# Kernel tuning notes

Hardware: AMD Instinct MI355X
Metric: run time of the kernel (lower is better)

Reference implementation:

```python
import jax, jax.numpy as jnp
import numpy as np

DIM = 1024
HEAD_DIM = 128
NUM_HEADS = 8
T = 8192
ATTN_SCALE = 0.1  # yarn.attn_scale after reset()
RMS_EPS = 1.1920929e-07  # torch F.rms_norm default eps for fp32


def setup_inputs() -> dict:
    key = jax.random.key(0)
    ks = jax.random.split(key, 6)
    x = jax.random.normal(ks[0], (1, T, DIM), jnp.float32)
    qkvo_w = jax.random.normal(ks[1], (4 * DIM, DIM), jnp.float32) * (DIM ** -0.5)
    ve = jax.random.normal(ks[2], (1, T, DIM), jnp.float32)
    sa_lambdas = jnp.array([0.9, 1.1], jnp.float32)
    attn_gate_w = jax.random.normal(ks[3], (NUM_HEADS, 12), jnp.float32) * 0.1
    ve_gate_w = jax.random.normal(ks[4], (NUM_HEADS, 12), jnp.float32) * 0.1
    # YaRN rotary factors, exactly as Yarn.reset()
    n_freq = HEAD_DIM // 4
    ang = (1.0 / 1024.0) ** jnp.linspace(0.0, 1.0, n_freq, dtype=jnp.float32)
    ang = jnp.repeat(ang, 2)                                   # [head_dim//2]
    ang = jnp.concatenate([ang, jnp.zeros(HEAD_DIM // 2, jnp.float32)])
    theta = jnp.arange(T, dtype=jnp.float32)[:, None] * ang[None, :]
    sign = jnp.where(jnp.arange(HEAD_DIM) % 2 == 1, -1.0, 1.0).astype(jnp.float32)
    factor1 = jnp.cos(theta)
    factor2 = jnp.sin(theta) * sign                            # odd lanes negated
    seqlens = jnp.array([0, 2048, 4096, 6144, 8192], jnp.int32)  # cu_seqlens
    return {"x": x, "qkvo_w": qkvo_w, "ve": ve, "sa_lambdas": sa_lambdas,
            "factor1": factor1, "factor2": factor2,
            "attn_gate_w": attn_gate_w, "ve_gate_w": ve_gate_w,
            "seqlens": seqlens, "bm_size": 128, "key_offset": 1}


def _rms_norm(x):
    return x * jax.lax.rsqrt(jnp.mean(x * x, axis=-1, keepdims=True) + RMS_EPS)


def _rotary(x, f1, f2):
    # x: [B, T, H, D]; pairwise flip of adjacent lanes, then f1*x + f2*flip(x)
    xf = x.reshape(*x.shape[:-1], x.shape[-1] // 2, 2)[..., ::-1].reshape(x.shape)
    return f1[None, :x.shape[1], None, :] * x + f2[None, :x.shape[1], None, :] * xf


def _windowed_varlen_attn(q, k, v, seqlens, bs, scale):
    # q,k,v: [T, H, D]; causal sliding window (bs left, 0 right), varlen via cu_seqlens.
    Tt, H, D = q.shape
    nb = Tt // bs
    pad = jnp.zeros((bs, H, D), q.dtype)
    kp = jnp.concatenate([pad, k], axis=0)
    vp = jnp.concatenate([pad, v], axis=0)
    idx = jnp.arange(nb)[:, None] * bs + jnp.arange(2 * bs)[None, :]   # [nb, 2bs] into padded
    kb, vb = kp[idx], vp[idx]                                          # [nb, 2bs, H, D]
    qb = q.reshape(nb, bs, H, D)
    gq = jnp.arange(Tt).reshape(nb, bs)                                # global query idx
    gk = idx - bs                                                      # global key idx (may be <0)
    seg = jnp.searchsorted(seqlens, jnp.arange(Tt), side='right')      # segment id per token
    sq = seg.reshape(nb, bs)
    sk = seg[jnp.clip(gk, 0, Tt - 1)]
    mask = ((gk[:, None, :] >= 0)
            & (gk[:, None, :] <= gq[:, :, None])
            & (gq[:, :, None] - gk[:, None, :] <= bs)
            & (sq[:, :, None] == sk[:, None, :]))                      # [nb, bs, 2bs]
    s = jnp.einsum('nqhd,nkhd->nhqk', qb, kb) * scale
    s = jnp.where(mask[:, None], s, -jnp.inf)
    p = jax.nn.softmax(s, axis=-1)
    return jnp.einsum('nhqk,nkhd->nqhd', p, vb).reshape(Tt, H, D)


def _forward(x, qkvo_w, ve, sa_lambdas, factor1, factor2, attn_gate_w, ve_gate_w,
             seqlens, bm_size, key_offset):
    B, Tt = x.shape[0], x.shape[1]
    H, D = NUM_HEADS, HEAD_DIM
    qkv = x @ (sa_lambdas[0] * qkvo_w[:3 * DIM]).T                    # [B, T, 3*dim]
    qkv = qkv.reshape(B, Tt, 3 * H, D)
    q, k, v = qkv[:, :, :H], qkv[:, :, H:2 * H], qkv[:, :, 2 * H:]
    q, k = _rms_norm(q), _rms_norm(k)
    q, k = _rotary(q, factor1, factor2), _rotary(k, factor1, factor2)
    if key_offset:
        hd2 = D // 2
        k_hi = jnp.concatenate([k[:, :1, :, hd2:], k[:, :-1, :, hd2:]], axis=1)
        k = jnp.concatenate([k[..., :hd2], k_hi], axis=-1)
    ve_gate = 2.0 * jax.nn.sigmoid(x[..., :12] @ ve_gate_w.T).reshape(B, Tt, H, 1)
    v = v + ve_gate * ve.reshape(B, Tt, H, D)
    y = _windowed_varlen_attn(q[0], k[0], v[0], seqlens, bm_size, ATTN_SCALE)
    y = y.reshape(B, Tt, H, D)
    y = y * jax.nn.sigmoid(x[..., :12] @ attn_gate_w.T).reshape(B, Tt, H, 1)
    y = y.reshape(B, Tt, H * D)
    return y @ (sa_lambdas[1] * qkvo_w[3 * DIM:]).T


def reference(x, qkvo_w, ve, sa_lambdas, factor1, factor2, attn_gate_w, ve_gate_w,
              seqlens, bm_size, key_offset):
    return _forward(x, qkvo_w, ve, sa_lambdas, factor1, factor2,
                    attn_gate_w, ve_gate_w, seqlens, bm_size, key_offset)
```

## Files before the change

### kernel.cpp

```cpp
#include <hip/hip_runtime.h>


#define TSEQ 8192
#define DIMM 1024
#define NHEAD 8
#define HD 128
#define ATTN_SCALE 0.1f
#define RMS_EPS 1.1920929e-07f

typedef __bf16 bfx2 __attribute__((ext_vector_type(2)));
typedef __bf16 bfx4 __attribute__((ext_vector_type(4)));
typedef __bf16 bfx8 __attribute__((ext_vector_type(8)));
typedef float f32x4 __attribute__((ext_vector_type(4)));
typedef short s16x4 __attribute__((ext_vector_type(4)));

#define GLDS16(g, l)                                                         \
  __builtin_amdgcn_global_load_lds(                                          \
      (const __attribute__((address_space(1))) void*)(g),                    \
      (__attribute__((address_space(3))) void*)(l), 16, 0, 0)

__device__ __forceinline__ float sig_(float z) { return 1.0f / (1.0f + __expf(-z)); }

__global__ void k_prep(const float4* __restrict__ x, const float4* __restrict__ w,
                       const float* __restrict__ lam, bfx4* __restrict__ xb,
                       bfx4* __restrict__ w1b, bfx4* __restrict__ w2b) {
  const int nx = TSEQ * DIMM / 4;
  const int nw = 4096 * 1024 / 4;
  const float l0 = lam[0], l1 = lam[1];
  int i = blockIdx.x * blockDim.x + threadIdx.x;
  int stride = gridDim.x * blockDim.x;
  for (; i < nx + nw; i += stride) {
    if (i < nx) {
      float4 v = x[i];
      bfx4 o;
      o[0] = (__bf16)v.x; o[1] = (__bf16)v.y; o[2] = (__bf16)v.z; o[3] = (__bf16)v.w;
      xb[i] = o;
    } else {
      int j = i - nx;
      int row = (j * 4) >> 10;
      float s = (row < 3 * DIMM) ? l0 : l1;
      float4 v = w[j];
      bfx4 o;
      o[0] = (__bf16)(s * v.x); o[1] = (__bf16)(s * v.y);
      o[2] = (__bf16)(s * v.z); o[3] = (__bf16)(s * v.w);
      if (row < 3 * DIMM) w1b[j] = o;
      else                w2b[j - 3 * DIMM * DIMM / 4] = o;
    }
  }
}

template <typename CT>
__global__ __launch_bounds__(256, 2) void k_gemm2b(const __bf16* __restrict__ A,
                                                   const __bf16* __restrict__ B,
                                                   CT* __restrict__ C,
                                                   int M, int N, int K) {
  __shared__ __align__(16) __bf16 ldsb[2][256 * 64];
  const int tid = threadIdx.x;
  const int wave = tid >> 6, lane = tid & 63;
  const int wm = wave >> 1, wn = wave & 1;
  const int lr = lane & 15, lg = lane >> 4;
  const int bm = blockIdx.x, bn = blockIdx.y;

  const int srow = tid >> 3;
  const int scol = ((tid & 7) ^ (srow & 7)) * 8;
  const __bf16* Ag = A + (size_t)(bm * 128 + srow) * K + scol;
  const __bf16* Bg = B + (size_t)(bn * 128 + srow) * K + scol;

  char* buf0 = (char*)&ldsb[0][0];
  char* buf1 = (char*)&ldsb[1][0];

  auto stage = [&](int kt, char* buf) {
#pragma unroll
    for (int L = 0; L < 4; L++)
      GLDS16(Ag + (size_t)(L * 32) * K + kt * 64, buf + L * 4096 + wave * 1024);
#pragma unroll
    for (int L = 0; L < 4; L++)
      GLDS16(Bg + (size_t)(L * 32) * K + kt * 64, buf + 16384 + L * 4096 + wave * 1024);
  };

  const int aoffs = (wm * 64 + lr) * 128;
  const int boffs = 16384 + (wn * 64 + lr) * 128;
  const int s0 = (lg ^ (lr & 7)) * 16;
  const int s1 = ((4 + lg) ^ (lr & 7)) * 16;

  f32x4 acc[4][4] = {};

#define VMC0() asm volatile("s_waitcnt vmcnt(0)" ::: "memory")
#define BAR() __builtin_amdgcn_s_barrier()

  stage(0, buf0);
  VMC0(); BAR();

  const int NT = K / 64;
  for (int t = 0; t < NT; t++) {
    char* cur = (t & 1) ? buf1 : buf0;
    char* nxt = (t & 1) ? buf0 : buf1;
    if (t + 1 < NT) stage(t + 1, nxt);
    bfx8 af[4][2], bfr[4][2];
#pragma unroll
    for (int f = 0; f < 4; f++) {
      const char* p = cur + aoffs + f * 2048;
      af[f][0] = *(const bfx8*)(p + s0);
      af[f][1] = *(const bfx8*)(p + s1);
    }
#pragma unroll
    for (int f = 0; f < 4; f++) {
      const char* p = cur + boffs + f * 2048;
      bfr[f][0] = *(const bfx8*)(p + s0);
      bfr[f][1] = *(const bfx8*)(p + s1);
    }
    __builtin_amdgcn_s_setprio(1);
#pragma unroll
    for (int i = 0; i < 4; i++)
#pragma unroll
      for (int j = 0; j < 4; j++) {
        acc[i][j] = __builtin_amdgcn_mfma_f32_16x16x32_bf16(af[i][0], bfr[j][0], acc[i][j], 0, 0, 0);
        acc[i][j] = __builtin_amdgcn_mfma_f32_16x16x32_bf16(af[i][1], bfr[j][1], acc[i][j], 0, 0, 0);
      }
    __builtin_amdgcn_s_setprio(0);
    VMC0(); BAR();
  }

  const int rbase = bm * 128 + wm * 64 + lg * 4;
  const int cbase = bn * 128 + wn * 64 + lr;
#pragma unroll
  for (int f = 0; f < 4; f++)
#pragma unroll
    for (int rr = 0; rr < 4; rr++) {
      size_t rowoff = (size_t)(rbase + f * 16 + rr) * N + cbase;
#pragma unroll
      for (int nf = 0; nf < 4; nf++) C[rowoff + nf * 16] = (CT)acc[f][nf][rr];
    }
#undef VMC0
#undef BAR
}

__global__ __launch_bounds__(512) void k_post(
    const __bf16* __restrict__ qkv, const float* __restrict__ x,
    const float* __restrict__ ve, const float* __restrict__ f1,
    const float* __restrict__ f2, const float* __restrict__ agw,
    const float* __restrict__ vgw, const int* __restrict__ koff_p,
    __bf16* __restrict__ qb, __bf16* __restrict__ kb,
    __bf16* __restrict__ vT, float* __restrict__ ag) {
  __shared__ float vg_lds[32][8];
  __shared__ __bf16 vtile[HD][36];
  const int t0 = blockIdx.x * 32;
  const int tid = threadIdx.x;
  const int h = tid >> 6, l = tid & 63;
  const int d0 = 2 * l;
  const int koff = *koff_p;

  if (tid < 256) {
    const int tl = tid >> 3, hh = tid & 7;
    const int t = t0 + tl;
    float za = 0.0f, zg = 0.0f;
#pragma unroll
    for (int j = 0; j < 12; j++) {
      float xv = x[(size_t)t * DIMM + j];
      za += xv * agw[hh * 12 + j];
      zg += xv * vgw[hh * 12 + j];
    }
    ag[(size_t)t * NHEAD + hh] = sig_(za);
    vg_lds[tl][hh] = 2.0f * sig_(zg);
  }

#pragma unroll 2
  for (int tl = 0; tl < 32; tl++) {
    const int t = t0 + tl;
    const size_t qoff = (size_t)t * (3 * DIMM) + h * HD;

    bfx2 qv = *(const bfx2*)&qkv[qoff + d0];
    bfx2 kv = *(const bfx2*)&qkv[qoff + DIMM + d0];
    float q0 = (float)qv[0], q1 = (float)qv[1];
    float k0 = (float)kv[0], k1 = (float)kv[1];

    float sq = q0 * q0 + q1 * q1;
    float sk = k0 * k0 + k1 * k1;
#pragma unroll
    for (int off = 32; off; off >>= 1) {
      sq += __shfl_xor(sq, off);
      sk += __shfl_xor(sk, off);
    }
    float rq = rsqrtf(sq * (1.0f / 128.0f) + RMS_EPS);
    float rk = rsqrtf(sk * (1.0f / 128.0f) + RMS_EPS);
    q0 *= rq; q1 *= rq; k0 *= rk; k1 *= rk;

    float2 cc = *(const float2*)&f1[(size_t)t * HD + d0];
    float2 ss = *(const float2*)&f2[(size_t)t * HD + d0];
    float rq0 = cc.x * q0 + ss.x * q1, rq1 = cc.y * q1 + ss.y * q0;
    float rk0 = cc.x * k0 + ss.x * k1, rk1 = cc.y * k1 + ss.y * k0;

    bfx2 qo; qo[0] = (__bf16)rq0; qo[1] = (__bf16)rq1;
    *(bfx2*)&qb[(size_t)t * DIMM + h * HD + d0] = qo;

    bfx2 ko2; ko2[0] = (__bf16)rk0; ko2[1] = (__bf16)rk1;
    const size_t kcol = (size_t)h * HD + d0;
    if (!koff || l < 32) {
      *(bfx2*)&kb[(size_t)t * DIMM + kcol] = ko2;
    } else {
      if (t + 1 < TSEQ) *(bfx2*)&kb[(size_t)(t + 1) * DIMM + kcol] = ko2;
      if (t == 0)       *(bfx2*)&kb[kcol] = ko2;
    }
  }
  __syncthreads();

  const int w = tid >> 6;
  const int dout = tid >> 2, tof = (tid & 3) * 8;
  for (int hh = 0; hh < 8; hh++) {
#pragma unroll
    for (int it = 0; it < 4; it++) {
      const int tl = w * 4 + it;
      const int t = t0 + tl;
      const size_t voff = (size_t)t * (3 * DIMM) + 2 * DIMM + hh * HD;
      float va = (float)qkv[voff + l];
      float vb = (float)qkv[voff + l + 64];
      float vea = ve[(size_t)t * DIMM + hh * HD + l];
      float veb = ve[(size_t)t * DIMM + hh * HD + l + 64];
      float gv = vg_lds[tl][hh];
      vtile[l][tl]      = (__bf16)(va + gv * vea);
      vtile[l + 64][tl] = (__bf16)(vb + gv * veb);
    }
    __syncthreads();
    {
      bfx4 a0 = *(const bfx4*)&vtile[dout][tof];
      bfx4 a1 = *(const bfx4*)&vtile[dout][tof + 4];
      bfx8 p0;
      p0[0] = a0[0]; p0[1] = a0[1]; p0[2] = a0[2]; p0[3] = a0[3];
      p0[4] = a1[0]; p0[5] = a1[1]; p0[6] = a1[2]; p0[7] = a1[3];
      *(bfx8*)&vT[(size_t)(hh * HD + dout) * TSEQ + t0 + tof] = p0;
    }
    __syncthreads();
  }
}

__global__ __launch_bounds__(512, 4) void k_attn3(
    const __bf16* __restrict__ qb, const __bf16* __restrict__ kb,
    const __bf16* __restrict__ vT, const float* __restrict__ ag,
    const int* __restrict__ sl, int ns, __bf16* __restrict__ yb) {
  __shared__ __align__(16) char kls[65536];
  const int n = blockIdx.x, h = blockIdx.y;
  const int tid = threadIdx.x;
  const int w = tid >> 6, l = tid & 63;
  const int lr = l & 15, lg = l >> 4;
  const int q0r = n * 128 + w * 16;
  const int kbase = q0r - 128;
  const int kbb = n * 128 - 128;
  const int q = q0r + lr;
  const int kfs = (q0r < 128) ? ((128 - q0r) >> 4) : 0;

  bfx8 qf[4];
#pragma unroll
  for (int ds = 0; ds < 4; ds++)
    qf[ds] = *(const bfx8*)&qb[(size_t)q * DIMM + h * HD + ds * 32 + lg * 8];

  int segs = 0;
  for (int i = 0; i < ns; i++) {
    int v = sl[i];
    segs = (v <= q) ? ((v > segs) ? v : segs) : segs;
  }
  int klo = q - 128;
  if (segs > klo) klo = segs;
  if (klo < 0) klo = 0;
  __builtin_amdgcn_sched_barrier(0);

  {
    const int rr_ = tid >> 4;
    const int slot = tid & 15;
#pragma unroll
    for (int r = 0; r < 8; r++) {
      const int rel = r * 32 + rr_;
      int grow = kbb + rel;
      grow = grow < 0 ? 0 : grow;
      const int slotp = slot ^ (rel & 15);
      GLDS16(kb + (size_t)grow * DIMM + h * HD + slotp * 8,
             kls + r * 8192 + w * 1024);
    }
  }

  __builtin_amdgcn_sched_barrier(0);
  asm volatile("s_waitcnt vmcnt(0)" ::: "memory");
  __builtin_amdgcn_sched_barrier(0);
  __builtin_amdgcn_s_barrier();

  const int kswz = lr << 4;
  f32x4 sf[9] = {};
#pragma unroll
  for (int kf = 0; kf < 9; kf++) {
    if (kf >= kfs) {
      const int relrow = w * 16 + kf * 16 + lr;
      const char* kp = kls + relrow * 256;
      bfx8 k0 = *(const bfx8*)(kp + ((lg * 16) ^ kswz));
      bfx8 k1 = *(const bfx8*)(kp + ((64 + lg * 16) ^ kswz));
      bfx8 k2 = *(const bfx8*)(kp + ((128 + lg * 16) ^ kswz));
      bfx8 k3 = *(const bfx8*)(kp + ((192 + lg * 16) ^ kswz));
      sf[kf] = __builtin_amdgcn_mfma_f32_16x16x32_bf16(k0, qf[0], sf[kf], 0, 0, 0);
      sf[kf] = __builtin_amdgcn_mfma_f32_16x16x32_bf16(k1, qf[1], sf[kf], 0, 0, 0);
      sf[kf] = __builtin_amdgcn_mfma_f32_16x16x32_bf16(k2, qf[2], sf[kf], 0, 0, 0);
      sf[kf] = __builtin_amdgcn_mfma_f32_16x16x32_bf16(k3, qf[3], sf[kf], 0, 0, 0);
    }
  }

#pragma unroll
  for (int kf = 0; kf < 9; kf++)
#pragma unroll
    for (int rr = 0; rr < 4; rr++) {
      int k = kbase + kf * 16 + lg * 4 + rr;
      bool valid = (k >= klo) && (k <= q);
      sf[kf][rr] = valid ? sf[kf][rr] * ATTN_SCALE : -1e30f;
    }

  float mx = -1e30f;
#pragma unroll
  for (int kf = 0; kf < 9; kf++)
#pragma unroll
    for (int rr = 0; rr < 4; rr++) mx = fmaxf(mx, sf[kf][rr]);
  mx = fmaxf(mx, __shfl_xor(mx, 16));
  mx = fmaxf(mx, __shfl_xor(mx, 32));

  float lsum = 0.0f;
#pragma unroll
  for (int kf = 0; kf < 9; kf++)
#pragma unroll
    for (int rr = 0; rr < 4; rr++) {
      float p = __expf(sf[kf][rr] - mx);
      sf[kf][rr] = p;
      lsum += p;
    }
  lsum += __shfl_xor(lsum, 16);
  lsum += __shfl_xor(lsum, 32);

  __builtin_amdgcn_s_barrier();

  {
    const int slot = l & 31;
#pragma unroll
    for (int r = 0; r < 8; r++) {
      const int d = r * 16 + w * 2 + (l >> 5);
      const int slotp = slot ^ (d & 15);
      int tsrc = kbb + slotp * 8;
      tsrc = tsrc < 0 ? 0 : tsrc;
      GLDS16(vT + (size_t)(h * HD + d) * TSEQ + tsrc,
             kls + r * 8192 + w * 1024);
    }
  }

  __builtin_amdgcn_sched_barrier(0);
  asm volatile("s_waitcnt vmcnt(0)" ::: "memory");
  __builtin_amdgcn_sched_barrier(0);
  __builtin_amdgcn_s_barrier();

  f32x4 o[8] = {};
#pragma unroll
  for (int kf = 0; kf < 9; kf++) {
    if (kf >= kfs) {
      bfx4 pc;
      pc[0] = (__bf16)sf[kf][0]; pc[1] = (__bf16)sf[kf][1];
      pc[2] = (__bf16)sf[kf][2]; pc[3] = (__bf16)sf[kf][3];
      s16x4 pb = *(s16x4*)&pc;
      const int tof = (w * 32 + kf * 32 + lg * 8) ^ kswz;
#pragma unroll
      for (int nf = 0; nf < 8; nf++) {
        s16x4 vf = *(const s16x4*)(kls + (nf * 16 + lr) * 512 + tof);
        o[nf] = __builtin_amdgcn_mfma_f32_16x16x16bf16_1k(vf, pb, o[nf], 0, 0, 0);
      }
    }
  }

  const float sc = ag[(size_t)q * NHEAD + h] / lsum;
#pragma unroll
  for (int nf = 0; nf < 8; nf++) {
    bfx4 st;
#pragma unroll
    for (int rr = 0; rr < 4; rr++) st[rr] = (__bf16)(o[nf][rr] * sc);
    *(bfx4*)&yb[(size_t)q * DIMM + h * HD + nf * 16 + lg * 4] = st;
  }
}

extern "C" void kernel_launch(void* const* d_in, const int* in_sizes, int n_in,
                              void* d_out, int out_size, void* d_ws, size_t ws_size,
                              hipStream_t stream) {
  const float* x   = (const float*)d_in[0];
  const float* qw  = (const float*)d_in[1];
  const float* ve  = (const float*)d_in[2];
  const float* lam = (const float*)d_in[3];
  const float* f1  = (const float*)d_in[4];
  const float* f2  = (const float*)d_in[5];
  const float* agw = (const float*)d_in[6];
  const float* vgw = (const float*)d_in[7];
  const int*   sl  = (const int*)d_in[8];
  const int    ns  = in_sizes[8];
  const int*   koff = (const int*)d_in[10];
  float* out = (float*)d_out;
  char* ws = (char*)d_ws;

  const size_t MB = 1024 * 1024;
  if (ws_size < 105 * MB) return;
  __bf16* xb   = (__bf16*)(ws);
  __bf16* w1b  = (__bf16*)(ws + 16 * MB);
  __bf16* w2b  = (__bf16*)(ws + 22 * MB);
  __bf16* qkvb = (__bf16*)(ws + 24 * MB);
  __bf16* qbuf = (__bf16*)(ws + 72 * MB);
  __bf16* kbuf = (__bf16*)(ws + 88 * MB);
  float*  ag   = (float*)(ws + 104 * MB);
  __bf16* vT   = xb;
  __bf16* ybuf = qkvb;

  k_prep<<<3072, 256, 0, stream>>>((const float4*)x, (const float4*)qw, lam,
                                   (bfx4*)xb, (bfx4*)w1b, (bfx4*)w2b);
  k_gemm2b<__bf16><<<dim3(TSEQ / 128, 3 * DIMM / 128), 256, 0, stream>>>(
      xb, w1b, qkvb, TSEQ, 3 * DIMM, DIMM);
  k_post<<<TSEQ / 32, 512, 0, stream>>>(qkvb, x, ve, f1, f2, agw, vgw, koff,
                                        qbuf, kbuf, vT, ag);
  k_attn3<<<dim3(TSEQ / 128, NHEAD), 512, 0, stream>>>(qbuf, kbuf, vT, ag, sl, ns, ybuf);
  k_gemm2b<float><<<dim3(TSEQ / 128, DIMM / 128), 256, 0, stream>>>(
      ybuf, w2b, out, TSEQ, DIMM, DIMM);
}
```

Baseline: 141.0 us.

## Split K and V LDS waits to overlap partial loads with MFMA compute

In the attention kernel, each wave now waits only on the first four of its eight async K row loads (vmcnt(4)) before computing QK^T on the tiles already resident, then waits for the rest. The PV product is split into two halves over head-dim chunks, so the first four V-transposed row groups are consumed while the rest are still arriving. The bf16 P fragments are also precomputed before the V load. This is meant to hide global-to-LDS latency behind MFMA work, at the cost of extra barriers and more live registers.

```diff
diff --git a/kernel.cpp b/kernel.cpp
--- a/kernel.cpp
+++ b/kernel.cpp
@@ -1,4 +1,5 @@
 #include <hip/hip_runtime.h>
+#include <type_traits>
 
 
 #define TSEQ 8192
@@ -247,6 +248,7 @@
   const int kbb = n * 128 - 128;
   const int q = q0r + lr;
   const int kfs = (q0r < 128) ? ((128 - q0r) >> 4) : 0;
+  const int klim = 8 - w;
 
   bfx8 qf[4];
 #pragma unroll
@@ -278,7 +280,7 @@
   }
 
   __builtin_amdgcn_sched_barrier(0);
-  asm volatile("s_waitcnt vmcnt(0)" ::: "memory");
+  asm volatile("s_waitcnt vmcnt(4)" ::: "memory");
   __builtin_amdgcn_sched_barrier(0);
   __builtin_amdgcn_s_barrier();
 
@@ -286,7 +288,7 @@
   f32x4 sf[9] = {};
 #pragma unroll
   for (int kf = 0; kf < 9; kf++) {
-    if (kf >= kfs) {
+    if (kf >= kfs && kf < klim) {
       const int relrow = w * 16 + kf * 16 + lr;
       const char* kp = kls + relrow * 256;
       bfx8 k0 = *(const bfx8*)(kp + ((lg * 16) ^ kswz));
@@ -300,6 +302,27 @@
     }
   }
 
+  __builtin_amdgcn_sched_barrier(0);
+  asm volatile("s_waitcnt vmcnt(0)" ::: "memory");
+  __builtin_amdgcn_sched_barrier(0);
+  __builtin_amdgcn_s_barrier();
+
+#pragma unroll
+  for (int kf = 0; kf < 9; kf++) {
+    if (kf >= kfs && kf >= klim) {
+      const int relrow = w * 16 + kf * 16 + lr;
+      const char* kp = kls + relrow * 256;
+      bfx8 k0 = *(const bfx8*)(kp + ((lg * 16) ^ kswz));
+      bfx8 k1 = *(const bfx8*)(kp + ((64 + lg * 16) ^ kswz));
+      bfx8 k2 = *(const bfx8*)(kp + ((128 + lg * 16) ^ kswz));
+      bfx8 k3 = *(const bfx8*)(kp + ((192 + lg * 16) ^ kswz));
+      sf[kf] = __builtin_amdgcn_mfma_f32_16x16x32_bf16(k0, qf[0], sf[kf], 0, 0, 0);
+      sf[kf] = __builtin_amdgcn_mfma_f32_16x16x32_bf16(k1, qf[1], sf[kf], 0, 0, 0);
+      sf[kf] = __builtin_amdgcn_mfma_f32_16x16x32_bf16(k2, qf[2], sf[kf], 0, 0, 0);
+      sf[kf] = __builtin_amdgcn_mfma_f32_16x16x32_bf16(k3, qf[3], sf[kf], 0, 0, 0);
+    }
+  }
+
 #pragma unroll
   for (int kf = 0; kf < 9; kf++)
 #pragma unroll
@@ -328,6 +351,15 @@
     }
   lsum += __shfl_xor(lsum, 16);
   lsum += __shfl_xor(lsum, 32);
+
+  s16x4 pb[9];
+#pragma unroll
+  for (int kf = 0; kf < 9; kf++) {
+    bfx4 pc;
+    pc[0] = (__bf16)sf[kf][0]; pc[1] = (__bf16)sf[kf][1];
+    pc[2] = (__bf16)sf[kf][2]; pc[3] = (__bf16)sf[kf][3];
+    pb[kf] = *(s16x4*)&pc;
+  }
 
   __builtin_amdgcn_s_barrier();
 
@@ -345,26 +377,34 @@
   }
 
   __builtin_amdgcn_sched_barrier(0);
+  asm volatile("s_waitcnt vmcnt(4)" ::: "memory");
+  __builtin_amdgcn_sched_barrier(0);
+  __builtin_amdgcn_s_barrier();
+
+  f32x4 o[8] = {};
+  auto pv_quad = [&](auto nf0c) {
+    constexpr int NF0 = decltype(nf0c)::value;
+#pragma unroll
+    for (int j = 0; j < 4; j++) {
+      const int drow = (NF0 + j) * 16 + lr;
+#pragma unroll
+      for (int kf = 0; kf < 9; kf++) {
+        if (kf >= kfs) {
+          const int tof = (w * 32 + kf * 32 + lg * 8) ^ kswz;
+          s16x4 vf = *(const s16x4*)(kls + drow * 512 + tof);
+          o[NF0 + j] = __builtin_amdgcn_mfma_f32_16x16x16bf16_1k(vf, pb[kf], o[NF0 + j], 0, 0, 0);
+        }
+      }
+    }
+  };
+  pv_quad(std::integral_constant<int, 0>{});
+
+  __builtin_amdgcn_sched_barrier(0);
   asm volatile("s_waitcnt vmcnt(0)" ::: "memory");
   __builtin_amdgcn_sched_barrier(0);
   __builtin_amdgcn_s_barrier();
 
-  f32x4 o[8] = {};
-#pragma unroll
-  for (int kf = 0; kf < 9; kf++) {
-    if (kf >= kfs) {
-      bfx4 pc;
-      pc[0] = (__bf16)sf[kf][0]; pc[1] = (__bf16)sf[kf][1];
-      pc[2] = (__bf16)sf[kf][2]; pc[3] = (__bf16)sf[kf][3];
-      s16x4 pb = *(s16x4*)&pc;
-      const int tof = (w * 32 + kf * 32 + lg * 8) ^ kswz;
-#pragma unroll
-      for (int nf = 0; nf < 8; nf++) {
-        s16x4 vf = *(const s16x4*)(kls + (nf * 16 + lr) * 512 + tof);
-        o[nf] = __builtin_amdgcn_mfma_f32_16x16x16bf16_1k(vf, pb, o[nf], 0, 0, 0);
-      }
-    }
-  }
+  pv_quad(std::integral_constant<int, 4>{});
 
   const float sc = ag[(size_t)q * NHEAD + h] / lsum;
 #pragma unroll
```

Result: no change. 141.2 us (+0.2%).

## Use 256x256-tile 8-wave GEMM with phased LDS pipeline for QKV projection

Applied to the files above, without the earlier changes.

Adds a new GEMM kernel with 256x256 output tiles, 512 threads and 128 KB of double-buffered LDS. It stages half-tiles with global_load_lds and splits each K step into four read/MFMA phases, with explicit barriers, waitcnt and setprio. The QKV projection now uses this kernel, aiming for more operand reuse per byte loaded and more overlap of loads with MFMA. In exchange the grid shrinks to 384 blocks with one block per CU, which risks poor CU occupancy and tail imbalance. The output projection still uses the old kernel.

```diff
diff --git a/kernel.cpp b/kernel.cpp
--- a/kernel.cpp
+++ b/kernel.cpp
@@ -50,6 +50,139 @@
 }
 
 template <typename CT>
+__global__ __launch_bounds__(512, 1) void k_gemm256(const __bf16* __restrict__ A,
+                                                    const __bf16* __restrict__ B,
+                                                    CT* __restrict__ C,
+                                                    int M, int N, int K) {
+  __shared__ __align__(16) char lds2[2][65536];
+  const int tid = threadIdx.x;
+  const int wave = tid >> 6, lane = tid & 63;
+  const int wm = wave >> 2, wn = wave & 3;
+  const int lr = lane & 15, lg = lane >> 4;
+  const int bm = blockIdx.x, bn = blockIdx.y;
+
+  const int srow = tid >> 3;
+  const int scol = ((tid & 7) ^ (srow & 7)) * 8;
+  const __bf16* Ag = A + (size_t)(bm * 256 + srow) * K + scol;
+  const __bf16* Bg = B + (size_t)(bn * 256 + srow) * K + scol;
+
+  const int NT2 = K / 128;
+
+  auto stageH = [&](int H) {
+    const int t = H >> 2, h = H & 3;
+    char* base = lds2[t & 1] + h * 16384;
+    const __bf16* G = (h & 1) ? Bg : Ag;
+    const int rowbase = (h >> 1) * 128;
+#pragma unroll
+    for (int L = 0; L < 2; L++)
+      GLDS16(G + (size_t)(rowbase + L * 64) * K + t * 64,
+             base + L * 8192 + srow * 128 + (tid & 7) * 16);
+  };
+
+  const int s0 = (lg ^ (lr & 7)) * 16;
+  const int s1 = ((4 + lg) ^ (lr & 7)) * 16;
+  const int aregion = wm ? 32768 : 0;
+  const int bregion = (wn >= 2) ? 49152 : 16384;
+  const int brow0 = (wn & 1) * 64;
+
+  f32x4 acc[8][4] = {};
+  bfx8 af[2][4][2], bf[2][2][2];
+
+  auto readA = [&](const char* buf, int ah) {
+#pragma unroll
+    for (int i = 0; i < 4; i++) {
+      const char* p = buf + aregion + ((ah * 4 + i) * 16 + lr) * 128;
+      af[ah][i][0] = *(const bfx8*)(p + s0);
+      af[ah][i][1] = *(const bfx8*)(p + s1);
+    }
+  };
+  auto readB = [&](const char* buf, int bh) {
+#pragma unroll
+    for (int jl = 0; jl < 2; jl++) {
+      const char* p = buf + bregion + (brow0 + (bh * 2 + jl) * 16 + lr) * 128;
+      bf[bh][jl][0] = *(const bfx8*)(p + s0);
+      bf[bh][jl][1] = *(const bfx8*)(p + s1);
+    }
+  };
+  auto mfmaQ = [&](int ah, int bh) {
+    __builtin_amdgcn_s_setprio(1);
+#pragma unroll
+    for (int i = 0; i < 4; i++)
+#pragma unroll
+      for (int jl = 0; jl < 2; jl++)
+#pragma unroll
+        for (int kk = 0; kk < 2; kk++)
+          acc[ah * 4 + i][bh * 2 + jl] = __builtin_amdgcn_mfma_f32_16x16x32_bf16(
+              af[ah][i][kk], bf[bh][jl][kk], acc[ah * 4 + i][bh * 2 + jl], 0, 0, 0);
+    __builtin_amdgcn_s_setprio(0);
+  };
+
+#define BAR() __builtin_amdgcn_s_barrier()
+#define LGKM0() do { asm volatile("s_waitcnt lgkmcnt(0)" ::: "memory"); \
+                     __builtin_amdgcn_sched_barrier(0); } while (0)
+#define VMC(n) do { asm volatile("s_waitcnt vmcnt(%0)" ::"i"(n) : "memory"); \
+                    __builtin_amdgcn_sched_barrier(0); } while (0)
+
+  auto phase = [&](const char* buf, int PH, int stH, int wait) {
+    if (PH == 0) { readA(buf, 0); readB(buf, 0); }
+    else if (PH == 1) { readA(buf, 1); }
+    else if (PH == 2) { readB(buf, 1); }
+    if (stH >= 0) stageH(stH);
+    BAR();
+    LGKM0();
+    mfmaQ((PH == 1 || PH == 3) ? 1 : 0, (PH >= 2) ? 1 : 0);
+    if (wait == 6) VMC(6);
+    else if (wait == -1) VMC(0);
+    BAR();
+  };
+
+  stageH(0); stageH(1); stageH(2); stageH(3);
+  VMC(4);
+  stageH(4); stageH(5); stageH(6);
+  VMC(6);
+  BAR();
+
+  const char* buf0 = lds2[0];
+  const char* buf1 = lds2[1];
+  for (int j = 0; j < NT2 - 1; j++) {
+    const int base = 8 * j + 7;
+    phase(buf0, 0, base + 0, 0);
+    phase(buf0, 1, base + 1, 0);
+    phase(buf0, 2, base + 2, 0);
+    phase(buf0, 3, base + 3, 6);
+    phase(buf1, 0, base + 4, 0);
+    phase(buf1, 1, base + 5, 0);
+    phase(buf1, 2, base + 6, 0);
+    phase(buf1, 3, base + 7, 6);
+  }
+  {
+    const int lastH = 8 * (NT2 - 1) + 7;
+    phase(buf0, 0, lastH, 0);
+    phase(buf0, 1, -1, 0);
+    phase(buf0, 2, -1, 0);
+    phase(buf0, 3, -1, -1);
+    phase(buf1, 0, -1, 0);
+    phase(buf1, 1, -1, 0);
+    phase(buf1, 2, -1, 0);
+    phase(buf1, 3, -1, 0);
+  }
+
+  const int rbase = bm * 256 + wm * 128 + lg * 4;
+  const int cbase = bn * 256 + wn * 64 + lr;
+#pragma unroll
+  for (int f = 0; f < 8; f++)
+#pragma unroll
+    for (int rr = 0; rr < 4; rr++) {
+      size_t rowoff = (size_t)(rbase + f * 16 + rr) * N + cbase;
+#pragma unroll
+      for (int nf = 0; nf < 4; nf++) C[rowoff + nf * 16] = (CT)acc[f][nf][rr];
+    }
+#undef BAR
+#undef LGKM0
+#undef VMC
+}
+
+template <typename CT>
 __global__ __launch_bounds__(256, 2) void k_gemm2b(const __bf16* __restrict__ A,
                                                    const __bf16* __restrict__ B,
                                                    CT* __restrict__ C,
@@ -407,7 +540,7 @@
 
   k_prep<<<3072, 256, 0, stream>>>((const float4*)x, (const float4*)qw, lam,
                                    (bfx4*)xb, (bfx4*)w1b, (bfx4*)w2b);
-  k_gemm2b<__bf16><<<dim3(TSEQ / 128, 3 * DIMM / 128), 256, 0, stream>>>(
+  k_gemm256<__bf16><<<dim3(TSEQ / 256, 3 * DIMM / 256), 512, 0, stream>>>(
       xb, w1b, qkvb, TSEQ, 3 * DIMM, DIMM);
   k_post<<<TSEQ / 32, 512, 0, stream>>>(qkvb, x, ve, f1, f2, agw, vgw, koff,
                                         qbuf, kbuf, vT, ag);
```

Result: slower. 161.3 us (+14.4%).
